# Kernel tuning notes

Measured on AMD Instinct MI355X. Metric: run time of the kernel, lower is better.

The kernel has to match this reference:

```python
import jax, jax.numpy as jnp
import numpy as np

B, N, D = 4, 2048, 512
H = 8
E = D // H  # head_size = 64


def setup_inputs() -> dict:
    key = jax.random.key(0)
    ks = jax.random.split(key, 7)
    x1 = jax.random.normal(ks[0], (B, N, D), dtype=jnp.float32)  # keys
    x2 = jax.random.normal(ks[1], (B, N, D), dtype=jnp.float32)  # queries
    v = jax.random.normal(ks[2], (B, N, D), dtype=jnp.float32)
    # Conv1d(kernel_size=1, bias=False) weights per head, squeezed to matrices.
    s = 0.02
    Wq = jax.random.normal(ks[3], (H, E, D), dtype=jnp.float32) * s  # [head, head_size, q_feat]
    Wk = jax.random.normal(ks[4], (H, E, D), dtype=jnp.float32) * s
    Wv = jax.random.normal(ks[5], (H, E, D), dtype=jnp.float32) * s
    Wo = jax.random.normal(ks[6], (H, D, E), dtype=jnp.float32) * s  # [head, out_size, head_size]
    return {"x1": x1, "x2": x2, "v": v, "Wq": Wq, "Wk": Wk, "Wv": Wv, "Wo": Wo}


def reference(x1, x2, v, Wq, Wk, Wv, Wo):
    # rep='identity': k = x1, q = x2
    # Per-head 1x1 conv projections, vectorized over heads.
    Qh = jnp.einsum('bnd,hed->bhne', x2, Wq)   # [B,H,N,E]
    Kh = jnp.einsum('bnd,hed->bhne', x1, Wk)
    Vh = jnp.einsum('bnd,hed->bhne', v, Wv)
    scale = jnp.sqrt(jnp.float32(E))
    scores = jnp.einsum('bhie,bhje->bhij', Qh, Kh) / scale  # [B,H,Nq,Nk]
    weights = jax.nn.softmax(scores, axis=-1)
    rep_h = jnp.einsum('bhij,bhje->bhie', weights, Vh)       # [B,H,Nq,E]
    # Per-head output projection, summed over heads (rep += output_layers[h](...)).
    out = jnp.einsum('bhie,hoe->bio', rep_h, Wo)             # [B,Nq,out_size]
    return out
```

## Files before the change

### kernel.cpp

```cpp
#include <hip/hip_runtime.h>
#include <math.h>

#define NN 2048
#define DD 512
#define HH 8
#define EE 64

typedef unsigned short u16;
typedef __attribute__((ext_vector_type(8))) short bf16x8;
typedef __attribute__((ext_vector_type(4))) float f32x4;

#define MFMA(a,b,c) __builtin_amdgcn_mfma_f32_16x16x32_bf16((a),(b),(c),0,0,0)

__device__ __forceinline__ float fexp2(float x){
#if __has_builtin(__builtin_amdgcn_exp2f)
  return __builtin_amdgcn_exp2f(x);
#else
  return exp2f(x);
#endif
}

__device__ __forceinline__ unsigned rnd1(float x){
  unsigned u = __float_as_uint(x);
  return (u + 0x7fffu + ((u >> 16) & 1u)) >> 16;
}
__device__ __forceinline__ unsigned pk2(float a, float b){
  return rnd1(a) | (rnd1(b) << 16);
}
__device__ __forceinline__ unsigned tpk2(float a, float b){
  return (__float_as_uint(a) >> 16) | (__float_as_uint(b) & 0xffff0000u);
}
union I4V { int4 i; bf16x8 v; };
__device__ __forceinline__ bf16x8 ld_frag(const u16* p){
  I4V u; u.i = *(const int4*)p; return u.v;
}
__device__ __forceinline__ bf16x8 mk_frag(int a, int b, int c, int d){
  I4V u; u.i = make_int4(a,b,c,d); return u.v;
}


__global__ __launch_bounds__(256) void pack_kernel(
    const float* __restrict__ x1, const float* __restrict__ x2,
    const float* __restrict__ vin,
    const float* __restrict__ Wq, const float* __restrict__ Wk,
    const float* __restrict__ Wv, const float* __restrict__ Wo,
    u16* __restrict__ xpk, u16* __restrict__ wpk, u16* __restrict__ wopk)
{
  __shared__ float lds[64][68];
  const int z = blockIdx.z;
  const int t = threadIdx.x;

  if (z < 12) {
    const int nt = blockIdx.x, dt = blockIdx.y, pb = z;
    const int p = pb >> 2, b = pb & 3;
    const float* X = (p == 0) ? x2 : (p == 1) ? x1 : vin;

    {
      const int r = t >> 2, c0 = (t & 3) * 16;
      const float* src = X + ((size_t)b * NN + nt * 64 + r) * DD + dt * 64 + c0;
      float4 f0 = ((const float4*)src)[0];
      float4 f1 = ((const float4*)src)[1];
      float4 f2 = ((const float4*)src)[2];
      float4 f3 = ((const float4*)src)[3];
      *(float4*)&lds[r][c0]      = f0;
      *(float4*)&lds[r][c0 + 4]  = f1;
      *(float4*)&lds[r][c0 + 8]  = f2;
      *(float4*)&lds[r][c0 + 12] = f3;
    }
    __syncthreads();

    const int lane = t & 63, w = t >> 6, jl = lane & 15, q = lane >> 4;
    #pragma unroll
    for (int kcl = 0; kcl < 2; ++kcl) {
      float4 fa = *(const float4*)&lds[w * 16 + jl][kcl * 32 + q * 8];
      float4 fb = *(const float4*)&lds[w * 16 + jl][kcl * 32 + q * 8 + 4];
      int4 pk = make_int4(pk2(fa.x, fa.y), pk2(fa.z, fa.w),
                          pk2(fb.x, fb.y), pk2(fb.z, fb.w));
      const int ng = nt * 4 + w, kc = dt * 2 + kcl;
      *(int4*)&xpk[((((size_t)pb * 128 + ng) * 16 + kc) * 64 + lane) * 8] = pk;
    }
  } else {
    const int zi = (z - 12) * 256 + blockIdx.y * 32 + blockIdx.x;
    const int gid = zi * 256 + t;
    const int seg = gid >> 15, tid = gid & 32767;
    const int lane = tid & 63, jl = lane & 15, q = lane >> 4;
    const int es = (tid >> 6) & 3, kc = (tid >> 8) & 15, hh = tid >> 12;

    if (seg < 3) {
      const float* Wsrc = (seg == 0) ? Wq : (seg == 1) ? Wk : Wv;
      const float s = (seg == 0) ? 0.18033688011112042f : 1.0f;
      const float* src = Wsrc + ((size_t)hh * 64 + es * 16 + jl) * DD + kc * 32 + q * 8;
      float4 fa = *(const float4*)src;
      float4 fb = *(const float4*)(src + 4);
      int4 pk = make_int4(pk2(fa.x*s, fa.y*s), pk2(fa.z*s, fa.w*s),
                          pk2(fb.x*s, fb.y*s), pk2(fb.z*s, fb.w*s));
      *(int4*)&wpk[(size_t)(((seg*8 + hh)*16 + kc)*4 + es)*512 + lane*8] = pk;
    } else {
      const int k = kc * 32 + q * 8;
      const float* src = Wo + ((size_t)(k >> 6) * DD + hh * 64 + es * 16 + jl) * EE + (k & 63);
      float4 fa = *(const float4*)src;
      float4 fb = *(const float4*)(src + 4);
      int4 pk = make_int4(pk2(fa.x, fa.y), pk2(fa.z, fa.w),
                          pk2(fb.x, fb.y), pk2(fb.z, fb.w));
      *(int4*)&wopk[(size_t)(((hh*16 + kc)*4 + es)*512) + lane*8] = pk;
    }
  }
}

__global__ __launch_bounds__(256) void qkvproj_kernel(
    const u16* __restrict__ xpk, const u16* __restrict__ wpk,
    u16* __restrict__ Qpk, u16* __restrict__ Kpk, u16* __restrict__ Vpk)
{
  const int t = threadIdx.x, w = t >> 6, lane = t & 63;
  const int jl = lane & 15, q = lane >> 4;
  const int bn = blockIdx.x, ph = blockIdx.y;
  const int b = bn >> 5, nt = bn & 31, p = ph >> 3, h = ph & 7;

  const u16* xb = xpk + (((size_t)(p * 4 + b) * 128 + nt * 4 + w) * 16) * 512;
  const u16* wb = wpk + (size_t)ph * 32768;

  f32x4 acc[4];
  #pragma unroll
  for (int i = 0; i < 4; ++i) acc[i] = (f32x4){0.f,0.f,0.f,0.f};

  #pragma unroll 4
  for (int kc = 0; kc < 16; ++kc) {
    bf16x8 xf = ld_frag(xb + kc * 512 + lane * 8);
    #pragma unroll
    for (int es = 0; es < 4; ++es) {
      bf16x8 wf = ld_frag(wb + (size_t)(kc * 4 + es) * 512 + lane * 8);
      acc[es] = MFMA(wf, xf, acc[es]);
    }
  }

  const int bh = b * 8 + h;
  if (p < 2) {
    u16* O = (p ? Kpk : Qpk) + (size_t)bh * 131072;
    const int ng = nt * 4 + w;
    #pragma unroll
    for (int es = 0; es < 4; ++es) {
      const int kh = es >> 1, qp = (es & 1) * 2 + (q >> 1), off = (q & 1) * 4;
      *(uint2*)&O[(size_t)((ng * 2 + kh) * 64 + qp * 16 + jl) * 8 + off] =
          make_uint2(pk2(acc[es][0], acc[es][1]), pk2(acc[es][2], acc[es][3]));
    }
  } else {
    u16* O = Vpk + (size_t)bh * 131072 + nt * 4096;
    const int jc = w >> 1, qp = (w & 1) * 2 + (jl >> 3), jj = jl & 7;
    #pragma unroll
    for (int es = 0; es < 4; ++es)
      #pragma unroll
      for (int r = 0; r < 4; ++r)
        O[(size_t)((jc * 4 + es) * 64 + qp * 16 + q * 4 + r) * 8 + jj] =
            (u16)rnd1(acc[es][r]);
  }
}

__global__ __launch_bounds__(256, 2) void attn_kernel(
    const u16* __restrict__ Qpk, const u16* __restrict__ Kpk,
    const u16* __restrict__ Vpk, u16* __restrict__ Rpk)
{
  __shared__ union {
    short P[4][64][76];
    float slab[2][64 * 65];
  } sh;
  __shared__ float lbuf[4][64];

  const int tid = threadIdx.x, w = tid >> 6, lane = tid & 63;
  const int jl = lane & 15, q = lane >> 4;
  const int bx = blockIdx.x;
  const int itile = bx >> 5;
  const int bh = bx & 31;
  const int b = bh >> 3, h = bh & 7;

  const u16* Qp = Qpk + ((size_t)bh * 128 + itile * 4) * 1024;
  bf16x8 qf[4][2];
  #pragma unroll
  for (int is = 0; is < 4; ++is) {
    qf[is][0] = ld_frag(Qp + is * 1024 + lane * 8);
    qf[is][1] = ld_frag(Qp + is * 1024 + 512 + lane * 8);
  }

  const u16* Kp = Kpk + (size_t)bh * 131072 + (size_t)w * 32768;
  const u16* Vp = Vpk + (size_t)bh * 131072 + (size_t)w * 32768;

  char* pw = (char*)&sh.P[0][0][0] + w * 9728 + jl * 152 + q * 8;
  const char* pr = (const char*)&sh.P[0][0][0] + w * 9728 + jl * 152 + q * 16;

  f32x4 acc[4][4];
  #pragma unroll
  for (int m = 0; m < 4; ++m)
    #pragma unroll
    for (int e = 0; e < 4; ++e) acc[m][e] = (f32x4){0.f,0.f,0.f,0.f};
  float lac[4] = {0.f, 0.f, 0.f, 0.f};

  bf16x8 kf[4][2];
  #pragma unroll
  for (int jm = 0; jm < 4; ++jm) {
    kf[jm][0] = ld_frag(Kp + jm * 1024 + lane * 8);
    kf[jm][1] = ld_frag(Kp + jm * 1024 + 512 + lane * 8);
  }

  for (int jt = 0; jt < 8; ++jt) {
    const u16* Vb = Vp + jt * 4096;
    bf16x8 vf[4][2];
    #pragma unroll
    for (int es = 0; es < 4; ++es) {
      vf[es][0] = ld_frag(Vb + es * 512 + lane * 8);
      vf[es][1] = ld_frag(Vb + 2048 + es * 512 + lane * 8);
    }
    #pragma unroll
    for (int jm = 0; jm < 4; ++jm) {
      #pragma unroll
      for (int is = 0; is < 4; ++is) {
        f32x4 c = (f32x4){0.f,0.f,0.f,0.f};
        c = MFMA(kf[jm][0], qf[is][0], c);
        c = MFMA(kf[jm][1], qf[is][1], c);
        float e0 = fexp2(c[0]), e1 = fexp2(c[1]);
        float e2 = fexp2(c[2]), e3 = fexp2(c[3]);
        lac[is] += (e0 + e1) + (e2 + e3);
        int2 pv; pv.x = tpk2(e0, e1); pv.y = tpk2(e2, e3);
        *(int2*)(pw + is * 2432 + jm * 32) = pv;
      }
    }
    {
      const u16* Kn = Kp + ((jt + 1) & 7) * 4096;
      #pragma unroll
      for (int jm = 0; jm < 4; ++jm) {
        kf[jm][0] = ld_frag(Kn + jm * 1024 + lane * 8);
        kf[jm][1] = ld_frag(Kn + jm * 1024 + 512 + lane * 8);
      }
    }
    #pragma unroll
    for (int m = 0; m < 4; ++m) {
      int2 a0 = *(const int2*)(pr + m * 2432);
      int2 a1 = *(const int2*)(pr + m * 2432 + 8);
      int2 a2 = *(const int2*)(pr + m * 2432 + 64);
      int2 a3 = *(const int2*)(pr + m * 2432 + 72);
      bf16x8 p0 = mk_frag(a0.x, a0.y, a1.x, a1.y);
      bf16x8 p1 = mk_frag(a2.x, a2.y, a3.x, a3.y);
      #pragma unroll
      for (int es = 0; es < 4; ++es) {
        acc[m][es] = MFMA(p0, vf[es][0], acc[m][es]);
        acc[m][es] = MFMA(p1, vf[es][1], acc[m][es]);
      }
    }
  }

  #pragma unroll
  for (int is = 0; is < 4; ++is) {
    float lv = lac[is];
    lv += __shfl_xor(lv, 16, 64);
    lv += __shfl_xor(lv, 32, 64);
    if (lane < 16) lbuf[w][is * 16 + lane] = lv;
  }
  __syncthreads();

  if (w >= 2) {
    float* s = sh.slab[w - 2];
    #pragma unroll
    for (int m = 0; m < 4; ++m)
      #pragma unroll
      for (int es = 0; es < 4; ++es)
        #pragma unroll
        for (int r = 0; r < 4; ++r)
          s[(m * 16 + q * 4 + r) * 65 + es * 16 + jl] = acc[m][es][r];
  }
  __syncthreads();
  if (w < 2) {
    const float* s = sh.slab[w];
    #pragma unroll
    for (int m = 0; m < 4; ++m)
      #pragma unroll
      for (int es = 0; es < 4; ++es)
        #pragma unroll
        for (int r = 0; r < 4; ++r)
          acc[m][es][r] += s[(m * 16 + q * 4 + r) * 65 + es * 16 + jl];
  }
  __syncthreads();
  if (w == 1) {
    float* s = sh.slab[0];
    #pragma unroll
    for (int m = 0; m < 4; ++m)
      #pragma unroll
      for (int es = 0; es < 4; ++es)
        #pragma unroll
        for (int r = 0; r < 4; ++r)
          s[(m * 16 + q * 4 + r) * 65 + es * 16 + jl] = acc[m][es][r];
  }
  __syncthreads();
  if (w == 0) {
    const float* s = sh.slab[0];
    #pragma unroll
    for (int m = 0; m < 4; ++m) {
      float il[4];
      #pragma unroll
      for (int r = 0; r < 4; ++r) {
        const int i = m * 16 + q * 4 + r;
        il[r] = 1.0f / (lbuf[0][i] + lbuf[1][i] + lbuf[2][i] + lbuf[3][i]);
      }
      const int rg = b * 128 + itile * 4 + m;
      #pragma unroll
      for (int es = 0; es < 4; ++es) {
        const int kc = h * 2 + (es >> 1);
        const int qp = (es & 1) * 2 + (jl >> 3), jj = jl & 7;
        #pragma unroll
        for (int r = 0; r < 4; ++r) {
          float val = (acc[m][es][r] + s[(m * 16 + q * 4 + r) * 65 + es * 16 + jl]) * il[r];
          Rpk[((size_t)rg * 16 + kc) * 512 + (size_t)(qp * 16 + q * 4 + r) * 8 + jj] =
              (u16)rnd1(val);
        }
      }
    }
  }
}

__global__ __launch_bounds__(256) void outproj_kernel(
    const u16* __restrict__ Rpk, const u16* __restrict__ wopk,
    float* __restrict__ out)
{
  const int t = threadIdx.x, w = t >> 6, lane = t & 63;
  const int jl = lane & 15, q = lane >> 4;
  const int rt = blockIdx.x, ot = blockIdx.y;
  const int rg = rt * 4 + w;

  f32x4 acc[4];
  #pragma unroll
  for (int i = 0; i < 4; ++i) acc[i] = (f32x4){0.f,0.f,0.f,0.f};

  #pragma unroll 4
  for (int kc = 0; kc < 16; ++kc) {
    bf16x8 bf = ld_frag(Rpk + ((size_t)rg * 16 + kc) * 512 + lane * 8);
    #pragma unroll
    for (int os = 0; os < 4; ++os) {
      bf16x8 wf = ld_frag(wopk + (size_t)((ot * 16 + kc) * 4 + os) * 512 + lane * 8);
      acc[os] = MFMA(wf, bf, acc[os]);
    }
  }

  #pragma unroll
  for (int os = 0; os < 4; ++os) {
    float4 o4 = make_float4(acc[os][0], acc[os][1], acc[os][2], acc[os][3]);
    *(float4*)&out[(size_t)(rt * 64 + w * 16 + jl) * DD + ot * 64 + os * 16 + q * 4] = o4;
  }
}

extern "C" void kernel_launch(void* const* d_in, const int* in_sizes, int n_in,
                              void* d_out, int out_size, void* d_ws, size_t ws_size,
                              hipStream_t stream)
{
  const float* x1 = (const float*)d_in[0];
  const float* x2 = (const float*)d_in[1];
  const float* vv = (const float*)d_in[2];
  const float* Wq = (const float*)d_in[3];
  const float* Wk = (const float*)d_in[4];
  const float* Wv = (const float*)d_in[5];
  const float* Wo = (const float*)d_in[6];
  float* out = (float*)d_out;

  char* W = (char*)d_ws;
  u16* wpk  = (u16*)(W);
  u16* wopk = (u16*)(W + 1572864);
  u16* xpk  = (u16*)(W + 2097152);
  u16* Qpk  = (u16*)(W + 27262976);
  u16* Kpk  = (u16*)(W + 35651584);
  u16* Vpk  = (u16*)(W + 44040192);
  u16* Rpk  = (u16*)(W + 52428800);

  pack_kernel   <<<dim3(32, 8, 14), 256, 0, stream>>>(x1, x2, vv, Wq, Wk, Wv, Wo,
                                                      xpk, wpk, wopk);
  qkvproj_kernel<<<dim3(128, 24), 256, 0, stream>>>(xpk, wpk, Qpk, Kpk, Vpk);
  attn_kernel   <<<dim3(1024), 256, 0, stream>>>(Qpk, Kpk, Vpk, Rpk);
  outproj_kernel<<<dim3(128, 8), 256, 0, stream>>>(Rpk, wopk, out);
}
```

Before: 189.3 us.

## Split attention work by query rows per wave instead of key ranges

Each wave now owns 16 query rows and sweeps all 2048 keys, where before the four waves split the key range and shared 64 query rows. This removes the cross-wave shared-memory reduction of accumulators and row sums, along with its several __syncthreads. It also shrinks per-thread accumulators and the shared P buffer, and drops the two-blocks-per-CU launch bound. In exchange, every wave streams the full K and V for its head, so K/V global/L2 traffic per block grows about fourfold, with less reuse per fragment load.

```diff
diff --git a/kernel.cpp b/kernel.cpp
--- a/kernel.cpp
+++ b/kernel.cpp
@@ -155,15 +155,11 @@
   }
 }
 
-__global__ __launch_bounds__(256, 2) void attn_kernel(
+__global__ __launch_bounds__(256) void attn_kernel(
     const u16* __restrict__ Qpk, const u16* __restrict__ Kpk,
     const u16* __restrict__ Vpk, u16* __restrict__ Rpk)
 {
-  __shared__ union {
-    short P[4][64][76];
-    float slab[2][64 * 65];
-  } sh;
-  __shared__ float lbuf[4][64];
+  __shared__ short P[4][16][72];
 
   const int tid = threadIdx.x, w = tid >> 6, lane = tid & 63;
   const int jl = lane & 15, q = lane >> 4;
@@ -171,27 +167,23 @@
   const int itile = bx >> 5;
   const int bh = bx & 31;
   const int b = bh >> 3, h = bh & 7;
-
-  const u16* Qp = Qpk + ((size_t)bh * 128 + itile * 4) * 1024;
-  bf16x8 qf[4][2];
-  #pragma unroll
-  for (int is = 0; is < 4; ++is) {
-    qf[is][0] = ld_frag(Qp + is * 1024 + lane * 8);
-    qf[is][1] = ld_frag(Qp + is * 1024 + 512 + lane * 8);
-  }
-
-  const u16* Kp = Kpk + (size_t)bh * 131072 + (size_t)w * 32768;
-  const u16* Vp = Vpk + (size_t)bh * 131072 + (size_t)w * 32768;
-
-  char* pw = (char*)&sh.P[0][0][0] + w * 9728 + jl * 152 + q * 8;
-  const char* pr = (const char*)&sh.P[0][0][0] + w * 9728 + jl * 152 + q * 16;
-
-  f32x4 acc[4][4];
-  #pragma unroll
-  for (int m = 0; m < 4; ++m)
-    #pragma unroll
-    for (int e = 0; e < 4; ++e) acc[m][e] = (f32x4){0.f,0.f,0.f,0.f};
-  float lac[4] = {0.f, 0.f, 0.f, 0.f};
+  const int ig = itile * 4 + w;
+
+  bf16x8 qf[2];
+  #pragma unroll
+  for (int kh = 0; kh < 2; ++kh)
+    qf[kh] = ld_frag(Qpk + (((size_t)bh * 128 + ig) * 2 + kh) * 512 + lane * 8);
+
+  const u16* Kp = Kpk + (size_t)bh * 131072;
+  const u16* Vp = Vpk + (size_t)bh * 131072;
+
+  char* pw = (char*)&P[0][0][0] + w * 2304 + jl * 144 + q * 8;
+  const char* pr = (const char*)&P[0][0][0] + w * 2304 + jl * 144 + q * 16;
+
+  f32x4 acc[4];
+  #pragma unroll
+  for (int es = 0; es < 4; ++es) acc[es] = (f32x4){0.f,0.f,0.f,0.f};
+  float lac = 0.f;
 
   bf16x8 kf[4][2];
   #pragma unroll
@@ -200,7 +192,7 @@
     kf[jm][1] = ld_frag(Kp + jm * 1024 + 512 + lane * 8);
   }
 
-  for (int jt = 0; jt < 8; ++jt) {
+  for (int jt = 0; jt < 32; ++jt) {
     const u16* Vb = Vp + jt * 4096;
     bf16x8 vf[4][2];
     #pragma unroll
@@ -210,106 +202,56 @@
     }
     #pragma unroll
     for (int jm = 0; jm < 4; ++jm) {
-      #pragma unroll
-      for (int is = 0; is < 4; ++is) {
-        f32x4 c = (f32x4){0.f,0.f,0.f,0.f};
-        c = MFMA(kf[jm][0], qf[is][0], c);
-        c = MFMA(kf[jm][1], qf[is][1], c);
-        float e0 = fexp2(c[0]), e1 = fexp2(c[1]);
-        float e2 = fexp2(c[2]), e3 = fexp2(c[3]);
-        lac[is] += (e0 + e1) + (e2 + e3);
-        int2 pv; pv.x = tpk2(e0, e1); pv.y = tpk2(e2, e3);
-        *(int2*)(pw + is * 2432 + jm * 32) = pv;
-      }
+      f32x4 c = (f32x4){0.f,0.f,0.f,0.f};
+      c = MFMA(kf[jm][0], qf[0], c);
+      c = MFMA(kf[jm][1], qf[1], c);
+      float e0 = fexp2(c[0]), e1 = fexp2(c[1]);
+      float e2 = fexp2(c[2]), e3 = fexp2(c[3]);
+      lac += (e0 + e1) + (e2 + e3);
+      int2 pv; pv.x = tpk2(e0, e1); pv.y = tpk2(e2, e3);
+      *(int2*)(pw + jm * 32) = pv;
     }
     {
-      const u16* Kn = Kp + ((jt + 1) & 7) * 4096;
+      const u16* Kn = Kp + ((jt + 1) & 31) * 4096;
       #pragma unroll
       for (int jm = 0; jm < 4; ++jm) {
         kf[jm][0] = ld_frag(Kn + jm * 1024 + lane * 8);
         kf[jm][1] = ld_frag(Kn + jm * 1024 + 512 + lane * 8);
       }
     }
-    #pragma unroll
-    for (int m = 0; m < 4; ++m) {
-      int2 a0 = *(const int2*)(pr + m * 2432);
-      int2 a1 = *(const int2*)(pr + m * 2432 + 8);
-      int2 a2 = *(const int2*)(pr + m * 2432 + 64);
-      int2 a3 = *(const int2*)(pr + m * 2432 + 72);
-      bf16x8 p0 = mk_frag(a0.x, a0.y, a1.x, a1.y);
-      bf16x8 p1 = mk_frag(a2.x, a2.y, a3.x, a3.y);
+    {
+      I4V u0, u1;
+      u0.i.x = *(const int*)(pr);       u0.i.y = *(const int*)(pr + 4);
+      u0.i.z = *(const int*)(pr + 8);   u0.i.w = *(const int*)(pr + 12);
+      u1.i.x = *(const int*)(pr + 64);  u1.i.y = *(const int*)(pr + 68);
+      u1.i.z = *(const int*)(pr + 72);  u1.i.w = *(const int*)(pr + 76);
+      bf16x8 p0 = u0.v, p1 = u1.v;
       #pragma unroll
       for (int es = 0; es < 4; ++es) {
-        acc[m][es] = MFMA(p0, vf[es][0], acc[m][es]);
-        acc[m][es] = MFMA(p1, vf[es][1], acc[m][es]);
+        acc[es] = MFMA(p0, vf[es][0], acc[es]);
+        acc[es] = MFMA(p1, vf[es][1], acc[es]);
       }
     }
   }
 
-  #pragma unroll
-  for (int is = 0; is < 4; ++is) {
-    float lv = lac[is];
-    lv += __shfl_xor(lv, 16, 64);
-    lv += __shfl_xor(lv, 32, 64);
-    if (lane < 16) lbuf[w][is * 16 + lane] = lv;
-  }
-  __syncthreads();
-
-  if (w >= 2) {
-    float* s = sh.slab[w - 2];
-    #pragma unroll
-    for (int m = 0; m < 4; ++m)
-      #pragma unroll
-      for (int es = 0; es < 4; ++es)
-        #pragma unroll
-        for (int r = 0; r < 4; ++r)
-          s[(m * 16 + q * 4 + r) * 65 + es * 16 + jl] = acc[m][es][r];
-  }
-  __syncthreads();
-  if (w < 2) {
-    const float* s = sh.slab[w];
-    #pragma unroll
-    for (int m = 0; m < 4; ++m)
-      #pragma unroll
-      for (int es = 0; es < 4; ++es)
-        #pragma unroll
-        for (int r = 0; r < 4; ++r)
-          acc[m][es][r] += s[(m * 16 + q * 4 + r) * 65 + es * 16 + jl];
-  }
-  __syncthreads();
-  if (w == 1) {
-    float* s = sh.slab[0];
-    #pragma unroll
-    for (int m = 0; m < 4; ++m)
-      #pragma unroll
-      for (int es = 0; es < 4; ++es)
-        #pragma unroll
-        for (int r = 0; r < 4; ++r)
-          s[(m * 16 + q * 4 + r) * 65 + es * 16 + jl] = acc[m][es][r];
-  }
-  __syncthreads();
-  if (w == 0) {
-    const float* s = sh.slab[0];
-    #pragma unroll
-    for (int m = 0; m < 4; ++m) {
-      float il[4];
-      #pragma unroll
-      for (int r = 0; r < 4; ++r) {
-        const int i = m * 16 + q * 4 + r;
-        il[r] = 1.0f / (lbuf[0][i] + lbuf[1][i] + lbuf[2][i] + lbuf[3][i]);
-      }
-      const int rg = b * 128 + itile * 4 + m;
-      #pragma unroll
-      for (int es = 0; es < 4; ++es) {
-        const int kc = h * 2 + (es >> 1);
-        const int qp = (es & 1) * 2 + (jl >> 3), jj = jl & 7;
-        #pragma unroll
-        for (int r = 0; r < 4; ++r) {
-          float val = (acc[m][es][r] + s[(m * 16 + q * 4 + r) * 65 + es * 16 + jl]) * il[r];
-          Rpk[((size_t)rg * 16 + kc) * 512 + (size_t)(qp * 16 + q * 4 + r) * 8 + jj] =
-              (u16)rnd1(val);
-        }
-      }
+  float lv = lac;
+  lv += __shfl_xor(lv, 16, 64);
+  lv += __shfl_xor(lv, 32, 64);
+  const float il = 1.0f / lv;
+  float ilr[4];
+  #pragma unroll
+  for (int r = 0; r < 4; ++r)
+    ilr[r] = __shfl(il, q * 4 + r, 64);
+
+  const int rg = b * 128 + ig;
+  #pragma unroll
+  for (int es = 0; es < 4; ++es) {
+    const int kk = es * 16 + jl;
+    const int kc = h * 2 + (kk >> 5), qp = (kk >> 3) & 3, jj = jl & 7;
+    #pragma unroll
+    for (int r = 0; r < 4; ++r) {
+      Rpk[((size_t)rg * 16 + kc) * 512 + (size_t)(qp * 16 + q * 4 + r) * 8 + jj] =
+          (u16)rnd1(acc[es][r] * ilr[r]);
     }
   }
 }
```

New measurement: 211.7 us. +11.8%, slower.
